# Optimization experiments

Hardware: AMD Instinct MI355X
Metric: run time of the kernel (lower is better)

## Reference

```python
import jax, jax.numpy as jnp
import numpy as np

D_MODEL = 1024
N_HEADS = 16
HEAD_DIM = D_MODEL // N_HEADS
B, S = 2, 2048


def setup_inputs() -> dict:
    key = jax.random.key(0)
    ks = jax.random.split(key, 10)
    lin = lambda k: jax.random.normal(k, (D_MODEL, D_MODEL), jnp.float32) / np.sqrt(D_MODEL)
    return {
        "x": jax.random.normal(ks[0], (B, S, D_MODEL), jnp.float32),
        "W_boundary": lin(ks[1]),
        "b_boundary": jax.random.normal(ks[2], (D_MODEL,), jnp.float32) * 0.02,
        "W_q": lin(ks[3]),
        "b_q": jax.random.normal(ks[4], (D_MODEL,), jnp.float32) * 0.02,
        "W_k": lin(ks[5]),
        "b_k": jax.random.normal(ks[6], (D_MODEL,), jnp.float32) * 0.02,
        "W_v": lin(ks[7]),
        "b_v": jax.random.normal(ks[8], (D_MODEL,), jnp.float32) * 0.02,
        "radial_weights": jax.random.normal(ks[9], (N_HEADS, 1, 1), jnp.float32),
        "tropical_scale": jnp.ones((1,), jnp.float32),
    }


def tropical_softmax(x, scale):
    # max-plus algebra softmax: subtract max, rescale, normalize with eps
    x = (x - jnp.max(x, axis=-1, keepdims=True)) * scale
    e = jnp.exp(x)
    return e / (jnp.sum(e, axis=-1, keepdims=True) + 1e-8)


def reference(x, W_boundary, b_boundary, W_q, b_q, W_k, b_k, W_v, b_v,
              radial_weights, tropical_scale):
    bsz, seq, _ = x.shape
    boundary = x @ W_boundary.T + b_boundary  # [B,S,D]

    def heads(W, b):  # [B,S,D] -> [B,H,S,hd]
        return (x @ W.T + b).reshape(bsz, seq, N_HEADS, HEAD_DIM).transpose(0, 2, 1, 3)

    q = heads(W_q, b_q)
    k = heads(W_k, b_k)
    v = heads(W_v, b_v)

    q = q * jax.nn.sigmoid(radial_weights)  # broadcast [H,1,1]

    scores = jnp.einsum("bhqd,bhkd->bhqk", q, k) / np.sqrt(HEAD_DIM).astype(np.float32)
    attn = tropical_softmax(scores, tropical_scale)  # [B,H,S,S]

    out = jnp.einsum("bhqk,bhkd->bhqd", attn, v)
    out = out.transpose(0, 2, 1, 3).reshape(bsz, seq, D_MODEL)
    out = out + boundary
    return (out, attn)
```

## Files before the change

### kernel.cpp

```cpp
#include <hip/hip_runtime.h>

#define DM 1024
#define NH 16
#define HD 64
#define BB 2
#define SS 2048
#define MTOT (BB*SS)
#define NTOT (4*DM)

typedef __attribute__((ext_vector_type(8))) short short8;
typedef __attribute__((ext_vector_type(4))) float f32x4;

#define MFMA(a,b,c) __builtin_amdgcn_mfma_f32_16x16x32_bf16((a),(b),(c),0,0,0)

__device__ inline unsigned short f2bf(float f) {
  union { float f; unsigned u; } v; v.f = f;
  unsigned r = v.u + 0x7FFFu + ((v.u >> 16) & 1u);
  return (unsigned short)(r >> 16);
}

__device__ inline void gload_lds16(const void* g, void* l) {
  void* gnc = const_cast<void*>(g);
  __builtin_amdgcn_global_load_lds(
      (__attribute__((address_space(1))) void*)gnc,
      (__attribute__((address_space(3))) void*)l, 16, 0, 0);
}

__global__ __launch_bounds__(256) void k_convert(
    const float* __restrict__ x, const float* __restrict__ w0,
    const float* __restrict__ w1, const float* __restrict__ w2,
    const float* __restrict__ w3,
    unsigned short* __restrict__ xb, unsigned short* __restrict__ wb) {
  const int T4 = (MTOT * DM) / 4;
  int stride = gridDim.x * blockDim.x;
  for (int i = blockIdx.x * blockDim.x + threadIdx.x; i < 2 * T4; i += stride) {
    const float* src; unsigned short* dst;
    if (i < T4) { src = x + (size_t)i * 4; dst = xb + (size_t)i * 4; }
    else {
      int flat = (i - T4) * 4;
      int sel = flat >> 20;
      int off = flat & ((1 << 20) - 1);
      const float* w = (sel == 0) ? w0 : (sel == 1) ? w1 : (sel == 2) ? w2 : w3;
      src = w + off; dst = wb + flat;
    }
    float4 v = *(const float4*)src;
    ushort4 o; o.x = f2bf(v.x); o.y = f2bf(v.y); o.z = f2bf(v.z); o.w = f2bf(v.w);
    *(ushort4*)dst = o;
  }
}

__global__ __launch_bounds__(256) void k_proj(
    const unsigned short* __restrict__ xb, const unsigned short* __restrict__ wb,
    const float* __restrict__ bbd, const float* __restrict__ bq,
    const float* __restrict__ bk, const float* __restrict__ bv,
    const float* __restrict__ radial,
    float* __restrict__ outbd,
    unsigned short* __restrict__ qb, unsigned short* __restrict__ kb,
    unsigned short* __restrict__ vb) {
  __shared__ unsigned short lsA[128 * 64];
  __shared__ unsigned short lsB[128 * 64];
  const int tid = threadIdx.x;
  const int wave = tid >> 6, lane = tid & 63;
  const int wr = wave >> 1, wc = wave & 1;
  const int lin = blockIdx.y * gridDim.x + blockIdx.x;
  const int swz = (lin & 7) * 128 + (lin >> 3);
  const int m0 = (swz >> 5) * 128, n0 = (swz & 31) * 128;
  const int ro = lane & 15, gg = lane >> 4;
  const int srow = lane >> 3;
  const int scol = (lane & 7) * 8;
  f32x4 acc[4][4] = {};
  for (int kt = 0; kt < DM / 64; ++kt) {
    __syncthreads();
    #pragma unroll
    for (int i = 0; i < 4; ++i) {
      int c = wave * 4 + i;
      const unsigned short* ga = xb + (size_t)(m0 + c * 8 + srow) * DM + kt * 64 + scol;
      gload_lds16(ga, (void*)(lsA + c * 512));
      const unsigned short* gb = wb + (size_t)(n0 + c * 8 + srow) * DM + kt * 64 + scol;
      gload_lds16(gb, (void*)(lsB + c * 512));
    }
    __syncthreads();
    #pragma unroll
    for (int ks = 0; ks < 2; ++ks) {
      short8 a[4], b[4];
      int ko = ks * 32 + gg * 8;
      #pragma unroll
      for (int r = 0; r < 4; ++r)
        a[r] = *(const short8*)&lsA[(wr * 64 + r * 16 + ro) * 64 + ko];
      #pragma unroll
      for (int c = 0; c < 4; ++c)
        b[c] = *(const short8*)&lsB[(wc * 64 + c * 16 + ro) * 64 + ko];
      #pragma unroll
      for (int r = 0; r < 4; ++r)
        #pragma unroll
        for (int c = 0; c < 4; ++c)
          acc[r][c] = MFMA(a[r], b[c], acc[r][c]);
    }
  }
  const int which = n0 >> 10;
  #pragma unroll
  for (int r = 0; r < 4; ++r) {
    const int mbase = m0 + wr * 64 + r * 16 + gg * 4;
    #pragma unroll
    for (int c = 0; c < 4; ++c) {
      const int n = n0 + wc * 64 + c * 16 + ro;
      const int nn = n & 1023;
      #pragma unroll
      for (int j = 0; j < 4; ++j) {
        const int m = mbase + j;
        float v = acc[r][c][j];
        if (which == 0) {
          outbd[(size_t)m * DM + nn] = v + bbd[nn];
        } else {
          const int h = nn >> 6, d = nn & 63;
          const int b2 = m >> 11, s = m & 2047;
          const size_t o = (((size_t)(b2 * NH + h)) * SS + s) * HD + d;
          if (which == 1) {
            float sg = 1.f / (1.f + __expf(-radial[h]));
            qb[o] = f2bf((v + bq[nn]) * sg);
          } else if (which == 2) {
            kb[o] = f2bf(v + bk[nn]);
          } else {
            vb[o] = f2bf(v + bv[nn]);
          }
        }
      }
    }
  }
}

__global__ __launch_bounds__(256) void k_vt(
    const unsigned short* __restrict__ vb, unsigned short* __restrict__ vt) {
  __shared__ unsigned short t[64][65];
  const int bh = blockIdx.y, st = blockIdx.x;
  const int tid = threadIdx.x;
  const int r = tid >> 2, c4 = (tid & 3) * 16;
  const unsigned short* src = vb + ((size_t)bh * SS + st * 64 + r) * HD + c4;
  #pragma unroll
  for (int i = 0; i < 16; i += 4) {
    ushort4 v = *(const ushort4*)(src + i);
    t[r][c4 + i + 0] = v.x; t[r][c4 + i + 1] = v.y;
    t[r][c4 + i + 2] = v.z; t[r][c4 + i + 3] = v.w;
  }
  __syncthreads();
  const int dd = tid >> 2, s4 = (tid & 3) * 16;
  unsigned short* dst = vt + ((size_t)bh * HD + dd) * SS + st * 64 + s4;
  #pragma unroll
  for (int i = 0; i < 16; i += 4) {
    ushort4 o;
    o.x = t[s4 + i + 0][dd]; o.y = t[s4 + i + 1][dd];
    o.z = t[s4 + i + 2][dd]; o.w = t[s4 + i + 3][dd];
    *(ushort4*)(dst + i) = o;
  }
}

__global__ __launch_bounds__(256) void k_attn_pv(
    const unsigned short* __restrict__ qb, const unsigned short* __restrict__ kb,
    const unsigned short* __restrict__ vt, const float* __restrict__ tsc,
    float* __restrict__ attn, float* __restrict__ out) {
  __shared__ unsigned short lk[2][64 * 64];
  __shared__ unsigned short lv[2][64 * 64];
  __shared__ __align__(16) unsigned short pt[4][16 * 64];
  const int bh = blockIdx.y, qt = blockIdx.x;
  const int tid = threadIdx.x, wave = tid >> 6, lane = tid & 63;
  const int ro = lane & 15, gg = lane >> 4;

  const unsigned short* kb_bh = kb + (size_t)bh * SS * HD;
  const unsigned short* vt_bh = vt + (size_t)bh * HD * SS;

  int sr0, sc0, sr1, sc1;
  {
    int s0 = (wave * 2 + 0) * 64 + lane;
    int s1 = (wave * 2 + 1) * 64 + lane;
    sr0 = s0 >> 3; sc0 = (s0 & 7) ^ (sr0 & 7);
    sr1 = s1 >> 3; sc1 = (s1 & 7) ^ (sr1 & 7);
  }

#define STAGE_K(buf, kt) do { \
    const unsigned short* g = kb_bh + (size_t)(kt) * 64 * HD; \
    gload_lds16(g + sr0 * 64 + sc0 * 8, (void*)(lk[buf] + (wave * 2 + 0) * 512)); \
    gload_lds16(g + sr1 * 64 + sc1 * 8, (void*)(lk[buf] + (wave * 2 + 1) * 512)); \
  } while (0)
#define STAGE_V(buf, kt) do { \
    const unsigned short* g = vt_bh + (size_t)(kt) * 64; \
    gload_lds16(g + (size_t)sr0 * SS + sc0 * 8, (void*)(lv[buf] + (wave * 2 + 0) * 512)); \
    gload_lds16(g + (size_t)sr1 * SS + sc1 * 8, (void*)(lv[buf] + (wave * 2 + 1) * 512)); \
  } while (0)

  STAGE_K(0, 0);

  const unsigned short* qrow =
      qb + ((size_t)bh * SS + qt * 64 + wave * 16 + ro) * HD;
  short8 aq0 = *(const short8*)(qrow + gg * 8);
  short8 aq1 = *(const short8*)(qrow + 32 + gg * 8);
  const float fac = tsc[0] * 0.125f;

  __syncthreads();

  float psum = 0.f;
  int cur = 0;
  for (int ct = 0; ct < 32; ++ct) {
    if (ct < 31) STAGE_K(cur ^ 1, ct + 1);
    const unsigned short* kbuf = lk[cur];
    #pragma unroll
    for (int sub = 0; sub < 4; ++sub) {
      const int rr = sub * 16 + ro;
      const unsigned short* kr = kbuf + rr * 64;
      short8 b0 = *(const short8*)&kr[(gg ^ (rr & 7)) * 8];
      short8 b1 = *(const short8*)&kr[((4 + gg) ^ (rr & 7)) * 8];
      f32x4 sf = {};
      sf = MFMA(b0, aq0, sf);
      sf = MFMA(b1, aq1, sf);
      psum += __expf(sf[0] * fac) + __expf(sf[1] * fac)
            + __expf(sf[2] * fac) + __expf(sf[3] * fac);
    }
    __syncthreads();
    cur ^= 1;
  }
  STAGE_K(0, 0);
  STAGE_V(0, 0);
  psum += __shfl_xor(psum, 16);
  psum += __shfl_xor(psum, 32);
  const float rsum = 1.f / (psum + 1e-8f);
  __syncthreads();

  float* ab = attn + ((size_t)bh * SS + qt * 64 + wave * 16 + ro) * SS;
  unsigned short* pw = &pt[wave][0];
  f32x4 acc[4] = {};
  cur = 0;
  for (int ct = 0; ct < 32; ++ct) {
    asm volatile("s_waitcnt vmcnt(4)" ::: "memory");
    __builtin_amdgcn_s_barrier();
    if (ct < 31) { STAGE_K(cur ^ 1, ct + 1); STAGE_V(cur ^ 1, ct + 1); }
    const unsigned short* kbuf = lk[cur];
    const unsigned short* vbuf = lv[cur];
    f32x4 st[4];
    #pragma unroll
    for (int sub = 0; sub < 4; ++sub) {
      const int rr = sub * 16 + ro;
      const unsigned short* kr = kbuf + rr * 64;
      short8 b0 = *(const short8*)&kr[(gg ^ (rr & 7)) * 8];
      short8 b1 = *(const short8*)&kr[((4 + gg) ^ (rr & 7)) * 8];
      f32x4 sf = {};
      sf = MFMA(b0, aq0, sf);
      sf = MFMA(b1, aq1, sf);
      st[sub][0] = __expf(sf[0] * fac) * rsum;
      st[sub][1] = __expf(sf[1] * fac) * rsum;
      st[sub][2] = __expf(sf[2] * fac) * rsum;
      st[sub][3] = __expf(sf[3] * fac) * rsum;
    }
    #pragma unroll
    for (int sub = 0; sub < 4; ++sub)
      __builtin_nontemporal_store(st[sub],
          (f32x4*)(ab + (ct * 4 + sub) * 16 + gg * 4));
    #pragma unroll
    for (int sub = 0; sub < 4; ++sub) {
      unsigned w0, w1;
      asm("v_cvt_pk_bf16_f32 %0, %1, %2" : "=v"(w0) : "v"(st[sub][0]), "v"(st[sub][1]));
      asm("v_cvt_pk_bf16_f32 %0, %1, %2" : "=v"(w1) : "v"(st[sub][2]), "v"(st[sub][3]));
      const int slot = (sub * 2 + (gg >> 1)) ^ (ro & 7);
      *(uint2*)((char*)pw + ro * 128 + slot * 16 + (gg & 1) * 8) = make_uint2(w0, w1);
    }
    #pragma unroll
    for (int ks = 0; ks < 2; ++ks) {
      const int pslot = (ks * 4 + gg) ^ (ro & 7);
      short8 pa = *(const short8*)((const char*)pw + ro * 128 + pslot * 16);
      #pragma unroll
      for (int dc = 0; dc < 4; ++dc) {
        const int rr = dc * 16 + ro;
        const int cc = (ks * 4 + gg) ^ (rr & 7);
        short8 bvf = *(const short8*)&vbuf[rr * 64 + cc * 8];
        acc[dc] = MFMA(pa, bvf, acc[dc]);
      }
    }
    cur ^= 1;
  }

  const int b2 = bh >> 4, h = bh & 15;
  const int s0 = qt * 64 + wave * 16 + gg * 4;
  #pragma unroll
  for (int dc = 0; dc < 4; ++dc)
    #pragma unroll
    for (int j = 0; j < 4; ++j) {
      size_t o = ((size_t)b2 * SS + s0 + j) * DM + h * HD + dc * 16 + ro;
      out[o] += acc[dc][j];
    }
#undef STAGE_K
#undef STAGE_V
}

extern "C" void kernel_launch(void* const* d_in, const int* in_sizes, int n_in,
                              void* d_out, int out_size, void* d_ws, size_t ws_size,
                              hipStream_t stream) {
  (void)in_sizes; (void)n_in; (void)out_size; (void)ws_size;
  const float* x   = (const float*)d_in[0];
  const float* Wb  = (const float*)d_in[1];
  const float* bb  = (const float*)d_in[2];
  const float* Wq  = (const float*)d_in[3];
  const float* bq  = (const float*)d_in[4];
  const float* Wk  = (const float*)d_in[5];
  const float* bk  = (const float*)d_in[6];
  const float* Wv  = (const float*)d_in[7];
  const float* bv  = (const float*)d_in[8];
  const float* rad = (const float*)d_in[9];
  const float* tsc = (const float*)d_in[10];

  float* out  = (float*)d_out;
  float* attn = out + (size_t)MTOT * DM;

  unsigned short* qb = (unsigned short*)d_ws;
  unsigned short* kb = qb + (size_t)4 * 1024 * 1024;
  unsigned short* vt = kb + (size_t)4 * 1024 * 1024;

  unsigned short* xb = (unsigned short*)attn;
  unsigned short* wb = xb + (size_t)4 * 1024 * 1024;
  unsigned short* vb = wb + (size_t)4 * 1024 * 1024;

  k_convert<<<2048, 256, 0, stream>>>(x, Wb, Wq, Wk, Wv, xb, wb);
  k_proj<<<dim3(32, 32), 256, 0, stream>>>(xb, wb, bb, bq, bk, bv, rad, out, qb, kb, vb);
  k_vt<<<dim3(32, 32), 256, 0, stream>>>(vb, vt);
  k_attn_pv<<<dim3(32, 32), 256, 0, stream>>>(qb, kb, vt, tsc, attn, out);
}
```

Measured before the change: 275.8 us.

## Software-pipeline QK^T of next chunk with PV of current chunk in attention pass

Restructures the second attention pass so the QK^T scores, exp and normalisation for chunk ct+1 are computed before the PV MFMAs of chunk ct. K is now staged two chunks ahead and V one chunk ahead, with the barrier moved to sit between the probability write and the next chunk's work. The goal is to overlap exp and score work with the PV matrix multiply and with the attention stores, hiding latency. In exchange it holds an extra set of score registers, which may raise register pressure. The K/V double-buffer indexing also becomes more intricate, so a staging mistake could introduce a race.

```diff
diff --git a/kernel.cpp b/kernel.cpp
--- a/kernel.cpp
+++ b/kernel.cpp
@@ -218,37 +218,39 @@
     cur ^= 1;
   }
   STAGE_K(0, 0);
+  STAGE_K(1, 1);
   STAGE_V(0, 0);
   psum += __shfl_xor(psum, 16);
   psum += __shfl_xor(psum, 32);
   const float rsum = 1.f / (psum + 1e-8f);
-  __syncthreads();
+  asm volatile("s_waitcnt vmcnt(0)" ::: "memory");
+  __builtin_amdgcn_s_barrier();
 
   float* ab = attn + ((size_t)bh * SS + qt * 64 + wave * 16 + ro) * SS;
   unsigned short* pw = &pt[wave][0];
   f32x4 acc[4] = {};
-  cur = 0;
+  f32x4 st[4], st2[4];
+
+#define QK_CHUNK(ct, stout) do { \
+    const unsigned short* kbuf = lk[(ct) & 1]; \
+    _Pragma("unroll") \
+    for (int sub = 0; sub < 4; ++sub) { \
+      const int rr = sub * 16 + ro; \
+      const unsigned short* kr = kbuf + rr * 64; \
+      short8 b0 = *(const short8*)&kr[(gg ^ (rr & 7)) * 8]; \
+      short8 b1 = *(const short8*)&kr[((4 + gg) ^ (rr & 7)) * 8]; \
+      f32x4 sf = {}; \
+      sf = MFMA(b0, aq0, sf); \
+      sf = MFMA(b1, aq1, sf); \
+      (stout)[sub][0] = __expf(sf[0] * fac) * rsum; \
+      (stout)[sub][1] = __expf(sf[1] * fac) * rsum; \
+      (stout)[sub][2] = __expf(sf[2] * fac) * rsum; \
+      (stout)[sub][3] = __expf(sf[3] * fac) * rsum; \
+    } \
+  } while (0)
+
+  QK_CHUNK(0, st);
   for (int ct = 0; ct < 32; ++ct) {
-    asm volatile("s_waitcnt vmcnt(4)" ::: "memory");
-    __builtin_amdgcn_s_barrier();
-    if (ct < 31) { STAGE_K(cur ^ 1, ct + 1); STAGE_V(cur ^ 1, ct + 1); }
-    const unsigned short* kbuf = lk[cur];
-    const unsigned short* vbuf = lv[cur];
-    f32x4 st[4];
-    #pragma unroll
-    for (int sub = 0; sub < 4; ++sub) {
-      const int rr = sub * 16 + ro;
-      const unsigned short* kr = kbuf + rr * 64;
-      short8 b0 = *(const short8*)&kr[(gg ^ (rr & 7)) * 8];
-      short8 b1 = *(const short8*)&kr[((4 + gg) ^ (rr & 7)) * 8];
-      f32x4 sf = {};
-      sf = MFMA(b0, aq0, sf);
-      sf = MFMA(b1, aq1, sf);
-      st[sub][0] = __expf(sf[0] * fac) * rsum;
-      st[sub][1] = __expf(sf[1] * fac) * rsum;
-      st[sub][2] = __expf(sf[2] * fac) * rsum;
-      st[sub][3] = __expf(sf[3] * fac) * rsum;
-    }
     #pragma unroll
     for (int sub = 0; sub < 4; ++sub)
       __builtin_nontemporal_store(st[sub],
@@ -261,6 +263,12 @@
       const int slot = (sub * 2 + (gg >> 1)) ^ (ro & 7);
       *(uint2*)((char*)pw + ro * 128 + slot * 16 + (gg & 1) * 8) = make_uint2(w0, w1);
     }
+    asm volatile("s_waitcnt vmcnt(4)" ::: "memory");
+    __builtin_amdgcn_s_barrier();
+    if (ct < 30) STAGE_K(ct & 1, ct + 2);
+    if (ct < 31) STAGE_V((ct + 1) & 1, ct + 1);
+    if (ct < 31) QK_CHUNK(ct + 1, st2);
+    const unsigned short* vbuf = lv[ct & 1];
     #pragma unroll
     for (int ks = 0; ks < 2; ++ks) {
       const int pslot = (ks * 4 + gg) ^ (ro & 7);
@@ -273,8 +281,10 @@
         acc[dc] = MFMA(pa, bvf, acc[dc]);
       }
     }
-    cur ^= 1;
-  }
+    #pragma unroll
+    for (int sub = 0; sub < 4; ++sub) st[sub] = st2[sub];
+  }
+#undef QK_CHUNK
 
   const int b2 = bh >> 4, h = bh & 15;
   const int s0 = qt * 64 + wave * 16 + gg * 4;
```

Measured after the change: 290.8 us. 5.4% more time.

## Split softmax row-sum pass into separate split-K kernel before attention-PV

Applied to the files above, without the earlier changes.

Moves the first pass (computing exp row sums over all keys) out of the attention kernel into a new kernel that splits the key range in two halves, doubling the grid to 2048 blocks. The attention kernel then reads the two partial sums instead of recomputing them, so it only does the normalized pass. This aims to raise parallelism and occupancy for the sum pass, at the cost of an extra launch and a small workspace round-trip.

```diff
diff --git a/kernel.cpp b/kernel.cpp
--- a/kernel.cpp
+++ b/kernel.cpp
@@ -154,9 +154,65 @@
   }
 }
 
+__global__ __launch_bounds__(256) void k_sum(
+    const unsigned short* __restrict__ qb, const unsigned short* __restrict__ kb,
+    const float* __restrict__ tsc, float* __restrict__ sums) {
+  __shared__ unsigned short lk[2][64 * 64];
+  const int half = blockIdx.x >> 5, qt = blockIdx.x & 31, bh = blockIdx.y;
+  const int tid = threadIdx.x, wave = tid >> 6, lane = tid & 63;
+  const int ro = lane & 15, gg = lane >> 4;
+  const unsigned short* kb_bh = kb + (size_t)bh * SS * HD;
+  int sr0, sc0, sr1, sc1;
+  {
+    int s0 = (wave * 2 + 0) * 64 + lane;
+    int s1 = (wave * 2 + 1) * 64 + lane;
+    sr0 = s0 >> 3; sc0 = (s0 & 7) ^ (sr0 & 7);
+    sr1 = s1 >> 3; sc1 = (s1 & 7) ^ (sr1 & 7);
+  }
+#define STAGE_K(buf, kt) do { \
+    const unsigned short* g = kb_bh + (size_t)(kt) * 64 * HD; \
+    gload_lds16(g + sr0 * 64 + sc0 * 8, (void*)(lk[buf] + (wave * 2 + 0) * 512)); \
+    gload_lds16(g + sr1 * 64 + sc1 * 8, (void*)(lk[buf] + (wave * 2 + 1) * 512)); \
+  } while (0)
+  STAGE_K(0, half * 16);
+  const unsigned short* qrow =
+      qb + ((size_t)bh * SS + qt * 64 + wave * 16 + ro) * HD;
+  short8 aq0 = *(const short8*)(qrow + gg * 8);
+  short8 aq1 = *(const short8*)(qrow + 32 + gg * 8);
+  const float fac = tsc[0] * 0.125f;
+  __syncthreads();
+  float psum = 0.f;
+  int cur = 0;
+  for (int i = 0; i < 16; ++i) {
+    const int ct = half * 16 + i;
+    if (i < 15) STAGE_K(cur ^ 1, ct + 1);
+    const unsigned short* kbuf = lk[cur];
+    #pragma unroll
+    for (int sub = 0; sub < 4; ++sub) {
+      const int rr = sub * 16 + ro;
+      const unsigned short* kr = kbuf + rr * 64;
+      short8 b0 = *(const short8*)&kr[(gg ^ (rr & 7)) * 8];
+      short8 b1 = *(const short8*)&kr[((4 + gg) ^ (rr & 7)) * 8];
+      f32x4 sf = {};
+      sf = MFMA(b0, aq0, sf);
+      sf = MFMA(b1, aq1, sf);
+      psum += __expf(sf[0] * fac) + __expf(sf[1] * fac)
+            + __expf(sf[2] * fac) + __expf(sf[3] * fac);
+    }
+    __syncthreads();
+    cur ^= 1;
+  }
+  psum += __shfl_xor(psum, 16);
+  psum += __shfl_xor(psum, 32);
+  if (lane < 16)
+    sums[(size_t)half * BB * NH * SS + (size_t)bh * SS + qt * 64 + wave * 16 + ro] = psum;
+#undef STAGE_K
+}
+
 __global__ __launch_bounds__(256) void k_attn_pv(
     const unsigned short* __restrict__ qb, const unsigned short* __restrict__ kb,
     const unsigned short* __restrict__ vt, const float* __restrict__ tsc,
+    const float* __restrict__ sums,
     float* __restrict__ attn, float* __restrict__ out) {
   __shared__ unsigned short lk[2][64 * 64];
   __shared__ unsigned short lv[2][64 * 64];
@@ -188,46 +244,23 @@
   } while (0)
 
   STAGE_K(0, 0);
-
-  const unsigned short* qrow =
-      qb + ((size_t)bh * SS + qt * 64 + wave * 16 + ro) * HD;
+  STAGE_V(0, 0);
+
+  const int row = qt * 64 + wave * 16 + ro;
+  const unsigned short* qrow = qb + ((size_t)bh * SS + row) * HD;
   short8 aq0 = *(const short8*)(qrow + gg * 8);
   short8 aq1 = *(const short8*)(qrow + 32 + gg * 8);
   const float fac = tsc[0] * 0.125f;
+  const float p0 = sums[(size_t)bh * SS + row];
+  const float p1 = sums[(size_t)BB * NH * SS + (size_t)bh * SS + row];
+  const float rsum = 1.f / (p0 + p1 + 1e-8f);
 
   __syncthreads();
 
-  float psum = 0.f;
-  int cur = 0;
-  for (int ct = 0; ct < 32; ++ct) {
-    if (ct < 31) STAGE_K(cur ^ 1, ct + 1);
-    const unsigned short* kbuf = lk[cur];
-    #pragma unroll
-    for (int sub = 0; sub < 4; ++sub) {
-      const int rr = sub * 16 + ro;
-      const unsigned short* kr = kbuf + rr * 64;
-      short8 b0 = *(const short8*)&kr[(gg ^ (rr & 7)) * 8];
-      short8 b1 = *(const short8*)&kr[((4 + gg) ^ (rr & 7)) * 8];
-      f32x4 sf = {};
-      sf = MFMA(b0, aq0, sf);
-      sf = MFMA(b1, aq1, sf);
-      psum += __expf(sf[0] * fac) + __expf(sf[1] * fac)
-            + __expf(sf[2] * fac) + __expf(sf[3] * fac);
-    }
-    __syncthreads();
-    cur ^= 1;
-  }
-  STAGE_K(0, 0);
-  STAGE_V(0, 0);
-  psum += __shfl_xor(psum, 16);
-  psum += __shfl_xor(psum, 32);
-  const float rsum = 1.f / (psum + 1e-8f);
-  __syncthreads();
-
-  float* ab = attn + ((size_t)bh * SS + qt * 64 + wave * 16 + ro) * SS;
+  float* ab = attn + ((size_t)bh * SS + row) * SS;
   unsigned short* pw = &pt[wave][0];
   f32x4 acc[4] = {};
-  cur = 0;
+  int cur = 0;
   for (int ct = 0; ct < 32; ++ct) {
     asm volatile("s_waitcnt vmcnt(4)" ::: "memory");
     __builtin_amdgcn_s_barrier();
@@ -311,6 +344,7 @@
   unsigned short* qb = (unsigned short*)d_ws;
   unsigned short* kb = qb + (size_t)4 * 1024 * 1024;
   unsigned short* vt = kb + (size_t)4 * 1024 * 1024;
+  float* sums = (float*)(vt + (size_t)4 * 1024 * 1024);
 
   unsigned short* xb = (unsigned short*)attn;
   unsigned short* wb = xb + (size_t)4 * 1024 * 1024;
@@ -319,5 +353,6 @@
   k_convert<<<2048, 256, 0, stream>>>(x, Wb, Wq, Wk, Wv, xb, wb);
   k_proj<<<dim3(32, 32), 256, 0, stream>>>(xb, wb, bb, bq, bk, bv, rad, out, qb, kb, vb);
   k_vt<<<dim3(32, 32), 256, 0, stream>>>(vb, vt);
-  k_attn_pv<<<dim3(32, 32), 256, 0, stream>>>(qb, kb, vt, tsc, attn, out);
-}
+  k_sum<<<dim3(64, 32), 256, 0, stream>>>(qb, kb, tsc, sums);
+  k_attn_pv<<<dim3(32, 32), 256, 0, stream>>>(qb, kb, vt, tsc, sums, attn, out);
+}
```

After: 299.6 us. 8.6% more time.
